# Kernel tuning notes

Hardware: AMD Instinct MI355X
Metric: run time of the kernel (lower is better)

## Reference

```python
import jax, jax.numpy as jnp
import numpy as np

IN_DIM, OUT_DIM, EDGE_DIM = 128, 128, 16
N_NODES, N_EDGES = 20000, 640000


def setup_inputs() -> dict:
    key = jax.random.key(0)
    ks = jax.random.split(key, 16)
    s = lambda fan_in: 1.0 / np.sqrt(fan_in)
    h = jax.random.normal(ks[0], (N_NODES, IN_DIM), dtype=jnp.float32)
    edge_index = jax.random.randint(ks[1], (2, N_EDGES), 0, N_NODES, dtype=jnp.int32)
    edge_attr = jax.random.normal(ks[2], (N_EDGES, EDGE_DIM), dtype=jnp.float32)
    flags = jnp.ones((N_NODES, 1), dtype=jnp.float32)
    edge_mask = jnp.ones((N_EDGES, 1), dtype=jnp.float32)
    din_msg = 2 * IN_DIM + EDGE_DIM
    din_node = IN_DIM + OUT_DIM
    params = {
        'W_m1': jax.random.uniform(ks[3], (din_msg, OUT_DIM), jnp.float32, -s(din_msg), s(din_msg)),
        'b_m1': jnp.zeros((OUT_DIM,), jnp.float32),
        'W_m2': jax.random.uniform(ks[4], (OUT_DIM, OUT_DIM), jnp.float32, -s(OUT_DIM), s(OUT_DIM)),
        'b_m2': jnp.zeros((OUT_DIM,), jnp.float32),
        'W_a': jax.random.uniform(ks[5], (OUT_DIM, 1), jnp.float32, -s(OUT_DIM), s(OUT_DIM)),
        'b_a': jnp.zeros((1,), jnp.float32),
        'W_n1': jax.random.uniform(ks[6], (din_node, OUT_DIM), jnp.float32, -s(din_node), s(din_node)),
        'b_n1': jnp.zeros((OUT_DIM,), jnp.float32),
        'W_n2': jax.random.uniform(ks[7], (OUT_DIM, OUT_DIM), jnp.float32, -s(OUT_DIM), s(OUT_DIM)),
        'b_n2': jnp.zeros((OUT_DIM,), jnp.float32),
    }
    return {'h': h, 'edge_index': edge_index, 'edge_attr': edge_attr,
            'flags': flags, 'edge_mask': edge_mask, **params}


def reference(h, edge_index, edge_attr, flags, edge_mask,
              W_m1, b_m1, W_m2, b_m2, W_a, b_a, W_n1, b_n1, W_n2, b_n2):
    row, col = edge_index[0], edge_index[1]
    # gather endpoints and run edge MLP
    msg = jnp.concatenate([h[row], h[col], edge_attr], axis=1)  # [E, 2*in+edge]
    msg = jax.nn.silu(msg @ W_m1 + b_m1)
    msg = jax.nn.silu(msg @ W_m2 + b_m2)                        # [E, out]
    att = jax.nn.sigmoid(msg @ W_a + b_a)                       # [E, 1]
    msg = msg * att * edge_mask
    # scatter-add into source nodes (aggregation 'sum', norm factor 1)
    agg = jax.ops.segment_sum(msg, row, num_segments=h.shape[0])  # [N, out]
    agg = jnp.concatenate([h, agg], axis=1)                       # [N, in+out]
    upd = jax.nn.silu(agg @ W_n1 + b_n1) @ W_n2 + b_n2
    return (h + upd) * flags
```

## Files before the change

### kernel.cpp

```cpp
#include <hip/hip_runtime.h>
#include <math.h>

#define E_TOT   640000
#define NN      20000
#define DIM     128
#define EDGE_DIM 16

typedef float f32x4 __attribute__((ext_vector_type(4)));
typedef float f32x2 __attribute__((ext_vector_type(2)));
typedef short s16x8 __attribute__((ext_vector_type(8)));
typedef unsigned u32x4 __attribute__((ext_vector_type(4)));
typedef __bf16 bfx8 __attribute__((ext_vector_type(8)));

__device__ __forceinline__ unsigned short f2bf(float f) {
    unsigned u = __builtin_bit_cast(unsigned, f);
    u += 0x7fffu + ((u >> 16) & 1u);
    return (unsigned short)(u >> 16);
}
__device__ __forceinline__ unsigned cvt_pk_bf16(float lo, float hi) {
    unsigned r;
    asm("v_cvt_pk_bf16_f32 %0, %1, %2" : "=v"(r) : "v"(lo), "v"(hi));
    return r;
}
__device__ __forceinline__ float bf_lo(unsigned u) {
    return __builtin_bit_cast(float, u << 16);
}
__device__ __forceinline__ float bf_hi(unsigned u) {
    return __builtin_bit_cast(float, u & 0xffff0000u);
}
__device__ __forceinline__ float fast_exp2(float x) {
    float r; asm("v_exp_f32 %0, %1" : "=v"(r) : "v"(x)); return r;
}
__device__ __forceinline__ float fast_rcp(float x) {
    float r; asm("v_rcp_f32 %0, %1" : "=v"(r) : "v"(x)); return r;
}
#define LOG2E 1.44269504f
__device__ __forceinline__ float silu_f(float x) {
    return x * fast_rcp(1.0f + fast_exp2(-LOG2E * x));
}
__device__ __forceinline__ float sigmoid_f(float x) {
    return fast_rcp(1.0f + fast_exp2(-LOG2E * x));
}

#define MFMA16(a, b, c) __builtin_amdgcn_mfma_f32_16x16x32_bf16( \
    __builtin_bit_cast(bfx8, (a)), __builtin_bit_cast(bfx8, (b)), (c), 0, 0, 0)

__device__ __forceinline__ void pack_w(const float* __restrict__ W,
                                       unsigned short* __restrict__ Wp,
                                       int K, int id) {
    int t   = id & 7;
    int pos = (id >> 3) & 127;
    int sg  = id >> 10;
    int qq = pos & 15, f = pos >> 4;
    int col = (f >> 1) * 32 + 2 * qq + (f & 1);
    int k = sg * 8 + t;
    Wp[id] = (k < K) ? f2bf(W[(size_t)k * DIM + col]) : (unsigned short)0;
}

__global__ void prep_all_kernel(const float* __restrict__ h,
                                unsigned short* __restrict__ h_bf,
                                const float* __restrict__ Wm1,
                                const float* __restrict__ Wm2,
                                const float* __restrict__ Wn1,
                                const float* __restrict__ Wn2,
                                unsigned short* __restrict__ W1rp,
                                unsigned short* __restrict__ W1cp,
                                unsigned short* __restrict__ W1ep,
                                unsigned short* __restrict__ W2p,
                                unsigned short* __restrict__ Wn1p,
                                unsigned short* __restrict__ Wn2p,
                                float* __restrict__ agg,
                                int* __restrict__ cnts) {
    const int blk = blockIdx.x;
    const int tid = threadIdx.x;
    if (blk < 2500) {
        int i = blk * 256 + tid;
        float4 v = reinterpret_cast<const float4*>(h)[i];
        unsigned short* d = h_bf + i * 4;
        d[0] = f2bf(v.x); d[1] = f2bf(v.y); d[2] = f2bf(v.z); d[3] = f2bf(v.w);
    } else if (blk < 2564) {
        pack_w(Wm1, W1rp, 128, (blk - 2500) * 256 + tid);
    } else if (blk < 2628) {
        pack_w(Wm1 + 128 * DIM, W1cp, 128, (blk - 2564) * 256 + tid);
    } else if (blk < 2644) {
        pack_w(Wm1 + 256 * DIM, W1ep, 16, (blk - 2628) * 256 + tid);
    } else if (blk < 2708) {
        pack_w(Wm2, W2p, 128, (blk - 2644) * 256 + tid);
    } else if (blk < 2836) {
        pack_w(Wn1, Wn1p, 256, (blk - 2708) * 256 + tid);
    } else if (blk < 2900) {
        pack_w(Wn2, Wn2p, 128, (blk - 2836) * 256 + tid);
    } else if (blk < 5400) {
        int i = (blk - 2900) * 256 + tid;
        reinterpret_cast<f32x4*>(agg)[i] = (f32x4)0.f;
    } else {
        int i = (blk - 5400) * 256 + tid;
        if (i < NN) cnts[i] = 0;
    }
}

__global__ __launch_bounds__(256, 4) void proj_kernel(
    const unsigned short* __restrict__ h_bf,
    const unsigned short* __restrict__ W1rp,
    const unsigned short* __restrict__ W1cp,
    unsigned* __restrict__ P1r, unsigned* __restrict__ P1c)
{
    const int tid  = threadIdx.x;
    const int wv   = tid >> 6;
    const int lane = tid & 63;
    const int q    = lane & 15;
    const int g    = lane >> 4;
    const int n0w  = blockIdx.x * 64 + wv * 16;
    const int nq   = n0w + q;
    const int nqc  = (nq < NN) ? nq : (NN - 1);

    s16x8 av[4];
    #pragma unroll
    for (int s = 0; s < 4; ++s)
        av[s] = *reinterpret_cast<const s16x8*>(
            h_bf + (size_t)nqc * DIM + s * 32 + g * 8);

    #pragma unroll
    for (int T = 0; T < 2; ++T) {
        const unsigned short* Wp = T ? W1cp : W1rp;
        unsigned* P = T ? P1c : P1r;
        f32x4 acc[8];
        #pragma unroll
        for (int f = 0; f < 8; ++f) acc[f] = (f32x4)0.f;
        #pragma unroll
        for (int s = 0; s < 4; ++s)
            #pragma unroll
            for (int f = 0; f < 8; ++f) {
                s16x8 b = *reinterpret_cast<const s16x8*>(
                    Wp + ((s * 4 + g) * DIM + f * 16 + q) * 8);
                acc[f] = MFMA16(av[s], b, acc[f]);
            }
        #pragma unroll
        for (int r = 0; r < 4; ++r) {
            int n = n0w + g * 4 + r;
            if (n < NN) {
                u32x4 o;
                #pragma unroll
                for (int a = 0; a < 4; ++a)
                    o[a] = cvt_pk_bf16(acc[2 * a][r], acc[2 * a + 1][r]);
                *reinterpret_cast<u32x4*>(P + (size_t)n * 64 + q * 4) = o;
            }
        }
    }
}

__global__ void hist_kernel(const int* __restrict__ ei, int* __restrict__ counts) {
    int e = blockIdx.x * blockDim.x + threadIdx.x;
    if (e < E_TOT) atomicAdd(&counts[ei[e]], 1);
}

__global__ __launch_bounds__(1024) void scan_kernel(int* __restrict__ counts) {
    __shared__ int s[1024];
    const int tid = threadIdx.x;
    const int CH = 20;
    int base = tid * CH;
    int loc[CH];
    int sum = 0;
    #pragma unroll
    for (int i = 0; i < CH; ++i) {
        int idx = base + i;
        loc[i] = (idx < NN) ? counts[idx] : 0;
        sum += loc[i];
    }
    s[tid] = sum;
    __syncthreads();
    for (int off = 1; off < 1024; off <<= 1) {
        int v = (tid >= off) ? s[tid - off] : 0;
        __syncthreads();
        s[tid] += v;
        __syncthreads();
    }
    int run = s[tid] - sum;
    #pragma unroll
    for (int i = 0; i < CH; ++i) {
        int idx = base + i;
        if (idx < NN) counts[idx] = run;
        run += loc[i];
    }
}

__global__ void scatter_kernel(const int* __restrict__ ei, int* __restrict__ cursor,
                               int* __restrict__ eidS, unsigned short* __restrict__ rowS) {
    int e = blockIdx.x * blockDim.x + threadIdx.x;
    if (e < E_TOT) {
        int r = ei[e];
        int p = atomicAdd(&cursor[r], 1);
        eidS[p] = e;
        rowS[p] = (unsigned short)r;
    }
}

template<bool SORTED>
__global__ __launch_bounds__(256, 2) void edge_kernel(
    const unsigned* __restrict__ P1r,
    const unsigned* __restrict__ P1c,
    const int* __restrict__ ei,
    const int* __restrict__ eidS,
    const unsigned short* __restrict__ rowS,
    const float* __restrict__ ea,
    const float* __restrict__ emask,
    const unsigned short* __restrict__ W1ep,
    const float* __restrict__ bm1,
    const unsigned short* __restrict__ W2p,
    const float* __restrict__ bm2,
    const float* __restrict__ Wa, const float* __restrict__ ba,
    float* __restrict__ agg)
{
    __shared__ __align__(16) unsigned char s_u[4][16384];

    const int tid  = threadIdx.x;
    const int wv   = tid >> 6;
    const int lane = tid & 63;
    const int q    = lane & 15;
    const int g    = lane >> 4;

    const int nwg = gridDim.x;
    const int xcd = blockIdx.x & 7;
    const int loc = blockIdx.x >> 3;
    const int qq  = nwg >> 3, rr = nwg & 7;
    const int tile = (xcd < rr) ? (xcd * (qq + 1) + loc)
                                : (rr * (qq + 1) + (xcd - rr) * qq + loc);
    const int e0w = tile * 256 + wv * 64;

    const int   eidl = SORTED ? eidS[e0w + lane] : (e0w + lane);
    const int   rowl = SORTED ? (int)rowS[e0w + lane] : ei[eidl];
    const int   coll = ei[E_TOT + eidl];
    const float mskl = emask[eidl];

    const u32x4* P1r4 = reinterpret_cast<const u32x4*>(P1r);
    const u32x4* P1c4 = reinterpret_cast<const u32x4*>(P1c);

    s16x8 eav[4];
    #pragma unroll
    for (int mi = 0; mi < 4; ++mi) {
        int eid = __shfl(eidl, mi * 16 + q);
        eav[mi] = (s16x8)0;
        if (g < 2) {
            const float4* pe = reinterpret_cast<const float4*>(
                ea + (size_t)eid * EDGE_DIM + g * 8);
            float4 u = pe[0], v = pe[1];
            u32x4 pk;
            pk[0] = cvt_pk_bf16(u.x, u.y); pk[1] = cvt_pk_bf16(u.z, u.w);
            pk[2] = cvt_pk_bf16(v.x, v.y); pk[3] = cvt_pk_bf16(v.z, v.w);
            eav[mi] = __builtin_bit_cast(s16x8, pk);
        }
    }

    s16x8 w1e[8];
    #pragma unroll
    for (int f = 0; f < 8; ++f)
        w1e[f] = *reinterpret_cast<const s16x8*>(
            W1ep + ((size_t)g * DIM + f * 16 + q) * 8);

    f32x2 b1v[4];
    #pragma unroll
    for (int a = 0; a < 4; ++a)
        b1v[a] = *reinterpret_cast<const f32x2*>(bm1 + a * 32 + 2 * q);

    unsigned char* sw = s_u[wv];

    u32x4 pr[4], pc[4];
    #pragma unroll
    for (int r = 0; r < 4; ++r) {
        int e = g * 4 + r;
        pr[r] = P1r4[(size_t)__shfl(rowl, e) * 16 + q];
        pc[r] = P1c4[(size_t)__shfl(coll, e) * 16 + q];
    }

    #pragma unroll
    for (int mi = 0; mi < 4; ++mi) {
        f32x4 a1[8];
        #pragma unroll
        for (int f = 0; f < 8; ++f) a1[f] = (f32x4)0.f;
        #pragma unroll
        for (int f = 0; f < 8; ++f) a1[f] = MFMA16(eav[mi], w1e[f], a1[f]);

        u32x4 prn[4], pcn[4];
        if (mi < 3) {
            #pragma unroll
            for (int r = 0; r < 4; ++r) {
                int e = (mi + 1) * 16 + g * 4 + r;
                prn[r] = P1r4[(size_t)__shfl(rowl, e) * 16 + q];
                pcn[r] = P1c4[(size_t)__shfl(coll, e) * 16 + q];
            }
        }

        #pragma unroll
        for (int r = 0; r < 4; ++r) {
            int e = mi * 16 + g * 4 + r;
            unsigned sx = (unsigned)((e & 7) << 4);
            #pragma unroll
            for (int a = 0; a < 4; ++a) {
                float v0 = a1[2 * a][r]     + bf_lo(pr[r][a]) + bf_lo(pc[r][a]) + b1v[a].x;
                float v1 = a1[2 * a + 1][r] + bf_hi(pr[r][a]) + bf_hi(pc[r][a]) + b1v[a].y;
                *reinterpret_cast<unsigned*>(
                    sw + e * 256 + ((a * 64 + q * 4) ^ sx)) =
                    cvt_pk_bf16(silu_f(v0), silu_f(v1));
            }
        }
        #pragma unroll
        for (int r = 0; r < 4; ++r) { pr[r] = prn[r]; pc[r] = pcn[r]; }
    }

    f32x4 acc2[4][8];
    #pragma unroll
    for (int mi = 0; mi < 4; ++mi)
        #pragma unroll
        for (int f = 0; f < 8; ++f) acc2[mi][f] = (f32x4)0.f;

    #pragma unroll
    for (int s = 0; s < 4; ++s) {
        s16x8 bf[8];
        #pragma unroll
        for (int f = 0; f < 8; ++f)
            bf[f] = *reinterpret_cast<const s16x8*>(
                W2p + ((s * 4 + g) * DIM + f * 16 + q) * 8);
        s16x8 av[4];
        #pragma unroll
        for (int mi = 0; mi < 4; ++mi) {
            int e = mi * 16 + q;
            av[mi] = *reinterpret_cast<const s16x8*>(
                sw + e * 256 + ((s * 64 + g * 16) ^ ((q & 7) << 4)));
        }
        #pragma unroll
        for (int mi = 0; mi < 4; ++mi)
            #pragma unroll
            for (int f = 0; f < 8; ++f) acc2[mi][f] = MFMA16(av[mi], bf[f], acc2[mi][f]);
    }

    unsigned* smsg = reinterpret_cast<unsigned*>(sw);
    {
        f32x2 b2v[4], wav[4];
        #pragma unroll
        for (int a = 0; a < 4; ++a) {
            b2v[a] = *reinterpret_cast<const f32x2*>(bm2 + a * 32 + 2 * q);
            wav[a] = *reinterpret_cast<const f32x2*>(Wa  + a * 32 + 2 * q);
        }
        const float ba0 = ba[0];
        #pragma unroll
        for (int mi = 0; mi < 4; ++mi)
            #pragma unroll
            for (int r = 0; r < 4; ++r) {
                float p = 0.f;
                #pragma unroll
                for (int a = 0; a < 4; ++a) {
                    float v0 = silu_f(acc2[mi][2 * a][r]     + b2v[a].x);
                    float v1 = silu_f(acc2[mi][2 * a + 1][r] + b2v[a].y);
                    acc2[mi][2 * a][r] = v0; acc2[mi][2 * a + 1][r] = v1;
                    p = fmaf(v0, wav[a].x, fmaf(v1, wav[a].y, p));
                }
                p += __shfl_xor(p, 1);
                p += __shfl_xor(p, 2);
                p += __shfl_xor(p, 4);
                p += __shfl_xor(p, 8);
                int e = mi * 16 + g * 4 + r;
                float mk = __shfl(mskl, e);
                float sc = sigmoid_f(p + ba0) * mk;
                unsigned sx = ((unsigned)(e & 4)) << 2;
                #pragma unroll
                for (int a = 0; a < 4; ++a) {
                    unsigned pk = cvt_pk_bf16(acc2[mi][2 * a][r] * sc,
                                              acc2[mi][2 * a + 1][r] * sc);
                    smsg[e * 64 + ((a * 16 + q) ^ sx)] = pk;
                }
            }
    }

    {
        const int c = lane;
        float s0 = 0.f, s1 = 0.f;
        int prow = __builtin_amdgcn_readlane(rowl, 0);
        for (int jb = 0; jb < 64; jb += 8) {
            unsigned v[8];
            #pragma unroll
            for (int k = 0; k < 8; ++k)
                v[k] = smsg[(jb + k) * 64 + (c ^ (((jb + k) & 4) << 2))];
            #pragma unroll
            for (int k = 0; k < 8; ++k) {
                int rj = __builtin_amdgcn_readlane(rowl, jb + k);
                if (rj != prow) {
                    float* dst = agg + (size_t)prow * DIM + (c >> 4) * 32 + 2 * (c & 15);
                    atomicAdd(dst, s0);
                    atomicAdd(dst + 1, s1);
                    s0 = 0.f; s1 = 0.f; prow = rj;
                }
                s0 += __builtin_bit_cast(float, v[k] << 16);
                s1 += __builtin_bit_cast(float, v[k] & 0xffff0000u);
            }
        }
        float* dst = agg + (size_t)prow * DIM + (c >> 4) * 32 + 2 * (c & 15);
        atomicAdd(dst, s0);
        atomicAdd(dst + 1, s1);
    }
}

__global__ __launch_bounds__(256, 4) void node_kernel(
    const unsigned short* __restrict__ h_bf,
    const float* __restrict__ agg,
    const float* __restrict__ h,
    const float* __restrict__ flags,
    const unsigned short* __restrict__ Wn1p,
    const float* __restrict__ bn1,
    const unsigned short* __restrict__ Wn2p,
    const float* __restrict__ bn2,
    float* __restrict__ out)
{
    __shared__ __align__(16) unsigned char s_u[4][4352];

    const int tid  = threadIdx.x;
    const int wv   = tid >> 6;
    const int lane = tid & 63;
    const int q    = lane & 15;
    const int g    = lane >> 4;
    const int n0w  = blockIdx.x * 64 + wv * 16;

    const int nq  = n0w + q;
    const int nqc = (nq < NN) ? nq : (NN - 1);

    f32x4 acc[8];
    #pragma unroll
    for (int f = 0; f < 8; ++f) acc[f] = (f32x4)0.f;

    #pragma unroll
    for (int s = 0; s < 4; ++s) {
        s16x8 a = *reinterpret_cast<const s16x8*>(
            h_bf + (size_t)nqc * DIM + s * 32 + g * 8);
        #pragma unroll
        for (int f = 0; f < 8; ++f) {
            s16x8 b = *reinterpret_cast<const s16x8*>(
                Wn1p + ((s * 4 + g) * DIM + f * 16 + q) * 8);
            acc[f] = MFMA16(a, b, acc[f]);
        }
    }
    #pragma unroll
    for (int s = 4; s < 8; ++s) {
        const float4* pa = reinterpret_cast<const float4*>(
            agg + (size_t)nqc * DIM + (s - 4) * 32 + g * 8);
        float4 u = pa[0], v = pa[1];
        u32x4 pk;
        pk[0] = cvt_pk_bf16(u.x, u.y); pk[1] = cvt_pk_bf16(u.z, u.w);
        pk[2] = cvt_pk_bf16(v.x, v.y); pk[3] = cvt_pk_bf16(v.z, v.w);
        s16x8 a = __builtin_bit_cast(s16x8, pk);
        #pragma unroll
        for (int f = 0; f < 8; ++f) {
            s16x8 b = *reinterpret_cast<const s16x8*>(
                Wn1p + ((s * 4 + g) * DIM + f * 16 + q) * 8);
            acc[f] = MFMA16(a, b, acc[f]);
        }
    }

    unsigned char* sw = s_u[wv];
    {
        #pragma unroll
        for (int aa = 0; aa < 4; ++aa) {
            f32x2 bp = *reinterpret_cast<const f32x2*>(bn1 + aa * 32 + 2 * q);
            #pragma unroll
            for (int r = 0; r < 4; ++r) {
                float v0 = silu_f(acc[2 * aa][r] + bp.x);
                float v1 = silu_f(acc[2 * aa + 1][r] + bp.y);
                *reinterpret_cast<unsigned*>(
                    sw + (g * 4 + r) * 272 + aa * 64 + 4 * q) = cvt_pk_bf16(v0, v1);
            }
        }
    }

    f32x4 acc2[8];
    #pragma unroll
    for (int f = 0; f < 8; ++f) acc2[f] = (f32x4)0.f;

    #pragma unroll
    for (int s = 0; s < 4; ++s) {
        s16x8 a = *reinterpret_cast<const s16x8*>(sw + q * 272 + s * 64 + g * 16);
        #pragma unroll
        for (int f = 0; f < 8; ++f) {
            s16x8 b = *reinterpret_cast<const s16x8*>(
                Wn2p + ((s * 4 + g) * DIM + f * 16 + q) * 8);
            acc2[f] = MFMA16(a, b, acc2[f]);
        }
    }

    {
        #pragma unroll
        for (int r = 0; r < 4; ++r) {
            int n = n0w + 4 * g + r;
            if (n < NN) {
                float fl = flags[n];
                #pragma unroll
                for (int aa = 0; aa < 4; ++aa) {
                    f32x2 b2 = *reinterpret_cast<const f32x2*>(bn2 + aa * 32 + 2 * q);
                    size_t b = (size_t)n * DIM + aa * 32 + 2 * q;
                    f32x2 hv = *reinterpret_cast<const f32x2*>(h + b);
                    f32x2 o;
                    o.x = (hv.x + acc2[2 * aa][r] + b2.x) * fl;
                    o.y = (hv.y + acc2[2 * aa + 1][r] + b2.y) * fl;
                    *reinterpret_cast<f32x2*>(out + b) = o;
                }
            }
        }
    }
}

extern "C" void kernel_launch(void* const* d_in, const int* in_sizes, int n_in,
                              void* d_out, int out_size, void* d_ws, size_t ws_size,
                              hipStream_t stream) {
    const float* h     = (const float*)d_in[0];
    const int*   ei    = (const int*)  d_in[1];
    const float* ea    = (const float*)d_in[2];
    const float* flags = (const float*)d_in[3];
    const float* emask = (const float*)d_in[4];
    const float* Wm1   = (const float*)d_in[5];
    const float* bm1   = (const float*)d_in[6];
    const float* Wm2   = (const float*)d_in[7];
    const float* bm2   = (const float*)d_in[8];
    const float* Wa    = (const float*)d_in[9];
    const float* ba    = (const float*)d_in[10];
    const float* Wn1   = (const float*)d_in[11];
    const float* bn1   = (const float*)d_in[12];
    const float* Wn2   = (const float*)d_in[13];
    const float* bn2   = (const float*)d_in[14];
    float* out = (float*)d_out;

    char* ws = (char*)d_ws;
    float*          agg   = (float*)         (ws);
    unsigned short* h_bf  = (unsigned short*)(ws + 10240000);
    unsigned short* W1rp  = (unsigned short*)(ws + 15360000);
    unsigned short* W1cp  = (unsigned short*)(ws + 15392768);
    unsigned short* W1ep  = (unsigned short*)(ws + 15425536);
    unsigned short* W2p   = (unsigned short*)(ws + 15433728);
    unsigned short* Wn1p  = (unsigned short*)(ws + 15466496);
    unsigned short* Wn2p  = (unsigned short*)(ws + 15532032);
    int*            cnts  = (int*)           (ws + 15564800);
    int*            eidS  = (int*)           (ws + 15644800);
    unsigned short* rowS  = (unsigned short*)(ws + 18204800);
    unsigned*       P1r   = (unsigned*)      (ws + 19484800);
    unsigned*       P1c   = (unsigned*)      (ws + 24604800);
    const size_t WS_NEED = 29724800;
    (void)WS_NEED;

    const bool sorted = (ws_size >= WS_NEED);

    prep_all_kernel<<<5479, 256, 0, stream>>>(h, h_bf, Wm1, Wm2, Wn1, Wn2,
                                              W1rp, W1cp, W1ep, W2p, Wn1p, Wn2p,
                                              agg, cnts);
    proj_kernel<<<(NN + 63) / 64, 256, 0, stream>>>(h_bf, W1rp, W1cp, P1r, P1c);

    if (sorted) {
        hist_kernel<<<(E_TOT + 255) / 256, 256, 0, stream>>>(ei, cnts);
        scan_kernel<<<1, 1024, 0, stream>>>(cnts);
        scatter_kernel<<<(E_TOT + 255) / 256, 256, 0, stream>>>(ei, cnts, eidS, rowS);
        edge_kernel<true><<<E_TOT / 256, 256, 0, stream>>>(
            P1r, P1c, ei, eidS, rowS, ea, emask, W1ep, bm1, W2p, bm2, Wa, ba, agg);
    } else {
        edge_kernel<false><<<E_TOT / 256, 256, 0, stream>>>(
            P1r, P1c, ei, eidS, rowS, ea, emask, W1ep, bm1, W2p, bm2, Wa, ba, agg);
    }

    node_kernel<<<(NN + 63) / 64, 256, 0, stream>>>(h_bf, agg, h, flags,
                                                    Wn1p, bn1, Wn2p, bn2, out);
}
```

Before: 239.7 us.

## Merge hist into prep, scatter into proj, memset zeroing, smaller edge blocks

```diff
diff --git a/kernel.cpp b/kernel.cpp
--- a/kernel.cpp
+++ b/kernel.cpp
@@ -57,20 +57,20 @@
     Wp[id] = (k < K) ? f2bf(W[(size_t)k * DIM + col]) : (unsigned short)0;
 }
 
-__global__ void prep_all_kernel(const float* __restrict__ h,
-                                unsigned short* __restrict__ h_bf,
-                                const float* __restrict__ Wm1,
-                                const float* __restrict__ Wm2,
-                                const float* __restrict__ Wn1,
-                                const float* __restrict__ Wn2,
-                                unsigned short* __restrict__ W1rp,
-                                unsigned short* __restrict__ W1cp,
-                                unsigned short* __restrict__ W1ep,
-                                unsigned short* __restrict__ W2p,
-                                unsigned short* __restrict__ Wn1p,
-                                unsigned short* __restrict__ Wn2p,
-                                float* __restrict__ agg,
-                                int* __restrict__ cnts) {
+__global__ void prep_hist_kernel(const float* __restrict__ h,
+                                 unsigned short* __restrict__ h_bf,
+                                 const float* __restrict__ Wm1,
+                                 const float* __restrict__ Wm2,
+                                 const float* __restrict__ Wn1,
+                                 const float* __restrict__ Wn2,
+                                 unsigned short* __restrict__ W1rp,
+                                 unsigned short* __restrict__ W1cp,
+                                 unsigned short* __restrict__ W1ep,
+                                 unsigned short* __restrict__ W2p,
+                                 unsigned short* __restrict__ Wn1p,
+                                 unsigned short* __restrict__ Wn2p,
+                                 const int* __restrict__ ei,
+                                 int* __restrict__ cnts) {
     const int blk = blockIdx.x;
     const int tid = threadIdx.x;
     if (blk < 2500) {
@@ -90,27 +90,71 @@
         pack_w(Wn1, Wn1p, 256, (blk - 2708) * 256 + tid);
     } else if (blk < 2900) {
         pack_w(Wn2, Wn2p, 128, (blk - 2836) * 256 + tid);
-    } else if (blk < 5400) {
-        int i = (blk - 2900) * 256 + tid;
-        reinterpret_cast<f32x4*>(agg)[i] = (f32x4)0.f;
     } else {
-        int i = (blk - 5400) * 256 + tid;
-        if (i < NN) cnts[i] = 0;
-    }
-}
-
-__global__ __launch_bounds__(256, 4) void proj_kernel(
+        int e = (blk - 2900) * 256 + tid;
+        if (e < E_TOT) atomicAdd(&cnts[ei[e]], 1);
+    }
+}
+
+__global__ __launch_bounds__(1024) void scan_kernel(int* __restrict__ counts) {
+    __shared__ int s[1024];
+    const int tid = threadIdx.x;
+    const int CH = 20;
+    int base = tid * CH;
+    int loc[CH];
+    int sum = 0;
+    #pragma unroll
+    for (int i = 0; i < CH; ++i) {
+        int idx = base + i;
+        loc[i] = (idx < NN) ? counts[idx] : 0;
+        sum += loc[i];
+    }
+    s[tid] = sum;
+    __syncthreads();
+    for (int off = 1; off < 1024; off <<= 1) {
+        int v = (tid >= off) ? s[tid - off] : 0;
+        __syncthreads();
+        s[tid] += v;
+        __syncthreads();
+    }
+    int run = s[tid] - sum;
+    #pragma unroll
+    for (int i = 0; i < CH; ++i) {
+        int idx = base + i;
+        if (idx < NN) counts[idx] = run;
+        run += loc[i];
+    }
+}
+
+template<bool SORTED>
+__global__ __launch_bounds__(256) void scatter_proj_kernel(
+    const int* __restrict__ ei, int* __restrict__ cursor,
+    int* __restrict__ eidS, unsigned short* __restrict__ rowS,
     const unsigned short* __restrict__ h_bf,
     const unsigned short* __restrict__ W1rp,
     const unsigned short* __restrict__ W1cp,
     unsigned* __restrict__ P1r, unsigned* __restrict__ P1c)
 {
-    const int tid  = threadIdx.x;
+    const int blk = blockIdx.x;
+    const int tid = threadIdx.x;
+
+    if (SORTED && blk < 2500) {
+        int e = blk * 256 + tid;
+        if (e < E_TOT) {
+            int r = ei[e];
+            int p = atomicAdd(&cursor[r], 1);
+            eidS[p] = e;
+            rowS[p] = (unsigned short)r;
+        }
+        return;
+    }
+
+    const int pblk = SORTED ? (blk - 2500) : blk;
     const int wv   = tid >> 6;
     const int lane = tid & 63;
     const int q    = lane & 15;
     const int g    = lane >> 4;
-    const int n0w  = blockIdx.x * 64 + wv * 16;
+    const int n0w  = pblk * 64 + wv * 16;
     const int nq   = n0w + q;
     const int nqc  = (nq < NN) ? nq : (NN - 1);
 
@@ -149,54 +193,8 @@
     }
 }
 
-__global__ void hist_kernel(const int* __restrict__ ei, int* __restrict__ counts) {
-    int e = blockIdx.x * blockDim.x + threadIdx.x;
-    if (e < E_TOT) atomicAdd(&counts[ei[e]], 1);
-}
-
-__global__ __launch_bounds__(1024) void scan_kernel(int* __restrict__ counts) {
-    __shared__ int s[1024];
-    const int tid = threadIdx.x;
-    const int CH = 20;
-    int base = tid * CH;
-    int loc[CH];
-    int sum = 0;
-    #pragma unroll
-    for (int i = 0; i < CH; ++i) {
-        int idx = base + i;
-        loc[i] = (idx < NN) ? counts[idx] : 0;
-        sum += loc[i];
-    }
-    s[tid] = sum;
-    __syncthreads();
-    for (int off = 1; off < 1024; off <<= 1) {
-        int v = (tid >= off) ? s[tid - off] : 0;
-        __syncthreads();
-        s[tid] += v;
-        __syncthreads();
-    }
-    int run = s[tid] - sum;
-    #pragma unroll
-    for (int i = 0; i < CH; ++i) {
-        int idx = base + i;
-        if (idx < NN) counts[idx] = run;
-        run += loc[i];
-    }
-}
-
-__global__ void scatter_kernel(const int* __restrict__ ei, int* __restrict__ cursor,
-                               int* __restrict__ eidS, unsigned short* __restrict__ rowS) {
-    int e = blockIdx.x * blockDim.x + threadIdx.x;
-    if (e < E_TOT) {
-        int r = ei[e];
-        int p = atomicAdd(&cursor[r], 1);
-        eidS[p] = e;
-        rowS[p] = (unsigned short)r;
-    }
-}
-
 template<bool SORTED>
-__global__ __launch_bounds__(256, 2) void edge_kernel(
+__global__ __launch_bounds__(128, 2) void edge_kernel(
     const unsigned* __restrict__ P1r,
     const unsigned* __restrict__ P1c,
     const int* __restrict__ ei,
@@ -211,7 +209,7 @@
     const float* __restrict__ Wa, const float* __restrict__ ba,
     float* __restrict__ agg)
 {
-    __shared__ __align__(16) unsigned char s_u[4][16384];
+    __shared__ __align__(16) unsigned char s_u[2][16384];
 
     const int tid  = threadIdx.x;
     const int wv   = tid >> 6;
@@ -225,7 +223,7 @@
     const int qq  = nwg >> 3, rr = nwg & 7;
     const int tile = (xcd < rr) ? (xcd * (qq + 1) + loc)
                                 : (rr * (qq + 1) + (xcd - rr) * qq + loc);
-    const int e0w = tile * 256 + wv * 64;
+    const int e0w = tile * 128 + wv * 64;
 
     const int   eidl = SORTED ? eidS[e0w + lane] : (e0w + lane);
     const int   rowl = SORTED ? (int)rowS[e0w + lane] : ei[eidl];
@@ -540,23 +538,26 @@
     unsigned*       P1r   = (unsigned*)      (ws + 19484800);
     unsigned*       P1c   = (unsigned*)      (ws + 24604800);
     const size_t WS_NEED = 29724800;
-    (void)WS_NEED;
 
     const bool sorted = (ws_size >= WS_NEED);
 
-    prep_all_kernel<<<5479, 256, 0, stream>>>(h, h_bf, Wm1, Wm2, Wn1, Wn2,
-                                              W1rp, W1cp, W1ep, W2p, Wn1p, Wn2p,
-                                              agg, cnts);
-    proj_kernel<<<(NN + 63) / 64, 256, 0, stream>>>(h_bf, W1rp, W1cp, P1r, P1c);
+    hipMemsetAsync(agg, 0, (size_t)NN * DIM * sizeof(float), stream);
+    hipMemsetAsync(cnts, 0, NN * sizeof(int), stream);
+
+    prep_hist_kernel<<<5400, 256, 0, stream>>>(h, h_bf, Wm1, Wm2, Wn1, Wn2,
+                                               W1rp, W1cp, W1ep, W2p, Wn1p, Wn2p,
+                                               ei, cnts);
 
     if (sorted) {
-        hist_kernel<<<(E_TOT + 255) / 256, 256, 0, stream>>>(ei, cnts);
         scan_kernel<<<1, 1024, 0, stream>>>(cnts);
-        scatter_kernel<<<(E_TOT + 255) / 256, 256, 0, stream>>>(ei, cnts, eidS, rowS);
-        edge_kernel<true><<<E_TOT / 256, 256, 0, stream>>>(
+        scatter_proj_kernel<true><<<2813, 256, 0, stream>>>(
+            ei, cnts, eidS, rowS, h_bf, W1rp, W1cp, P1r, P1c);
+        edge_kernel<true><<<E_TOT / 128, 128, 0, stream>>>(
             P1r, P1c, ei, eidS, rowS, ea, emask, W1ep, bm1, W2p, bm2, Wa, ba, agg);
     } else {
-        edge_kernel<false><<<E_TOT / 256, 256, 0, stream>>>(
+        scatter_proj_kernel<false><<<313, 256, 0, stream>>>(
+            ei, cnts, eidS, rowS, h_bf, W1rp, W1cp, P1r, P1c);
+        edge_kernel<false><<<E_TOT / 128, 128, 0, stream>>>(
             P1r, P1c, ei, eidS, rowS, ea, emask, W1ep, bm1, W2p, bm2, Wa, ba, agg);
     }
 
```

After: 254.6 us. 1.06x slower.
